# Performance work log

Hardware: AMD Instinct MI355X
Metric: run time of the kernel (lower is better)

The kernel has to match this reference:

```python
import jax, jax.numpy as jnp
import numpy as np

D = 512
V = 32000
T = 2048
B = 4
R = 8          # n_rules
STEPS = 5      # ca_steps
GATE_SCALE = 0.001  # gate_mode='micro'
EPS = 1e-5


def _layer_norm(x, g, b):
    m = jnp.mean(x, axis=-1, keepdims=True)
    v = jnp.mean((x - m) ** 2, axis=-1, keepdims=True)
    return (x - m) * jax.lax.rsqrt(v + EPS) * g + b


def setup_inputs() -> dict:
    key = jax.random.key(0)
    ks = jax.random.split(key, 16)
    s_in = 1.0 / np.sqrt(3 * D)
    s_h = 1.0 / np.sqrt(2 * D)
    s_d = 1.0 / np.sqrt(D)
    return {
        "tokens": jax.random.randint(ks[0], (B, T), 0, V, dtype=jnp.int64),
        "gate_signal": jax.random.normal(ks[1], (1, T, D), dtype=jnp.float32),
        "embed": jax.random.normal(ks[2], (V, D), dtype=jnp.float32),
        "pos_embed": jax.random.normal(ks[3], (T, D), dtype=jnp.float32),
        "rule_w1": jax.random.normal(ks[4], (R, 3 * D, 2 * D), dtype=jnp.float32) * s_in,
        "rule_b1": jnp.zeros((R, 2 * D), dtype=jnp.float32),
        "rule_w2": jax.random.normal(ks[5], (R, 2 * D, D), dtype=jnp.float32) * s_h,
        "rule_b2": jnp.zeros((R, D), dtype=jnp.float32),
        "sel_w": jax.random.normal(ks[6], (D, R), dtype=jnp.float32) * s_d,
        "sel_b": jnp.zeros((R,), dtype=jnp.float32),
        "norm_g": jnp.ones((STEPS, D), dtype=jnp.float32),
        "norm_b": jnp.zeros((STEPS, D), dtype=jnp.float32),
        "lnf_g": jnp.ones((D,), dtype=jnp.float32),
        "lnf_b": jnp.zeros((D,), dtype=jnp.float32),
        "head_w": jax.random.normal(ks[7], (D, V), dtype=jnp.float32) * s_d,
    }


def reference(tokens, gate_signal, embed, pos_embed, rule_w1, rule_b1,
              rule_w2, rule_b2, sel_w, sel_b, norm_g, norm_b,
              lnf_g, lnf_b, head_w):
    # x = token embed + positional embed  -> [B,T,D]
    x = embed[tokens] + pos_embed[None, :, :]

    # rule selector: step-invariant in 'micro' mode -> [T,R]
    logits = (gate_signal[0] * GATE_SCALE) @ sel_w + sel_b
    rw = jax.nn.softmax(logits, axis=-1)  # [T,R]

    for step in range(STEPS):
        x_left = jnp.roll(x, 1, axis=1)   # cat([x[:,-1:], x[:,:-1]])
        x_right = jnp.roll(x, -1, axis=1)  # cat([x[:,1:], x[:,:1]])
        nb = jnp.concatenate([x, x_left, x_right], axis=-1)  # [B,T,3D]
        # all R rule MLPs batched
        h = jnp.einsum('btk,rkh->btrh', nb, rule_w1) + rule_b1  # [B,T,R,2D]
        h = jax.nn.gelu(h, approximate=False)
        ro = jnp.einsum('btrh,rhd->btrd', h, rule_w2) + rule_b2  # [B,T,R,D]
        evolved = jnp.einsum('btrd,tr->btd', ro, rw)
        x = _layer_norm(x + evolved, norm_g[step], norm_b[step])

    return _layer_norm(x, lnf_g, lnf_b) @ head_w  # [B,T,V]
```

## Files before the change

kernel.cpp:

```cpp
#include <hip/hip_runtime.h>

#define T_SEQ 2048
#define BT    8192
#define DM    512
#define NR    8
#define NSTEP 5
#define K1    1536
#define H2    1024
#define VSZ   32000
#define HN    8192

using ushort_t = unsigned short;
using bf16x8 = __attribute__((ext_vector_type(8))) __bf16;
using f32x4  = __attribute__((ext_vector_type(4))) float;

__device__ __forceinline__ ushort_t f2bf(float f) {
    union { float f; unsigned u; } v; v.f = f;
    unsigned r = v.u + 0x7FFFu + ((v.u >> 16) & 1u);
    return (ushort_t)(r >> 16);
}

__device__ __forceinline__ float bf2f(unsigned hi) {
    union { unsigned u; float f; } v; v.u = hi << 16;
    return v.f;
}

__device__ __forceinline__ void gload16(const void* g, void* l) {
    __builtin_amdgcn_global_load_lds((const __attribute__((address_space(1))) void*)g,
                                     (__attribute__((address_space(3))) void*)l, 16, 0, 0);
}

__device__ __forceinline__ float gelu_fast(float x) {
    float x2 = x * x;
    float u  = x * fmaf(x2, 0.10294456f, 2.3022861f);
    float e  = exp2f(-u);
    return x * __builtin_amdgcn_rcpf(1.0f + e);
}

#define BAR()    __builtin_amdgcn_s_barrier()
#define VMCNT4() asm volatile("s_waitcnt vmcnt(4)" ::: "memory")
#define VMCNT0() asm volatile("s_waitcnt vmcnt(0)" ::: "memory")

__global__ void transpose_f32_bf16(const float* __restrict__ src, ushort_t* __restrict__ dst,
                                   int K, int N, long long srcBatch, long long dstBatch, int dstRow)
{
    __shared__ float tile[32][33];
    src += (size_t)blockIdx.z * srcBatch;
    dst += (size_t)blockIdx.z * dstBatch;
    int n0 = blockIdx.x * 32, k0 = blockIdx.y * 32;
    int tx = threadIdx.x, ty = threadIdx.y;
    #pragma unroll
    for (int i = 0; i < 32; i += 8)
        tile[ty + i][tx] = src[(size_t)(k0 + ty + i) * N + (n0 + tx)];
    __syncthreads();
    #pragma unroll
    for (int i = 0; i < 32; i += 8)
        dst[(size_t)(n0 + ty + i) * dstRow + (k0 + tx)] = f2bf(tile[tx][ty + i]);
}

__global__ void embed_pos(const int* __restrict__ tokens, const float* __restrict__ emb,
                          const float* __restrict__ pos, float* __restrict__ x,
                          ushort_t* __restrict__ xbf)
{
    int row = blockIdx.x;
    int t = row & (T_SEQ - 1);
    int tok = tokens[row];
    int i = threadIdx.x;
    float2 e = ((const float2*)(emb + (size_t)tok * DM))[i];
    float2 p = ((const float2*)(pos + (size_t)t * DM))[i];
    float2 v = make_float2(e.x + p.x, e.y + p.y);
    ((float2*)(x + (size_t)row * DM))[i] = v;
    ushort_t bb[2] = { f2bf(v.x), f2bf(v.y) };
    ((unsigned*)(xbf + (size_t)row * DM))[i] = *(const unsigned*)bb;
}

__global__ void rw_kernel(const float* __restrict__ gate, const float* __restrict__ selw,
                          const float* __restrict__ selb, const float* __restrict__ b2,
                          float* __restrict__ rw, float* __restrict__ b2rw)
{
    int t = blockIdx.x, lane = threadIdx.x;
    float p[NR];
    #pragma unroll
    for (int r = 0; r < NR; ++r) p[r] = 0.f;
    for (int d = lane; d < DM; d += 64) {
        float gv = gate[(size_t)t * DM + d] * 0.001f;
        const float* swr = selw + (size_t)d * NR;
        #pragma unroll
        for (int r = 0; r < NR; ++r) p[r] += gv * swr[r];
    }
    #pragma unroll
    for (int o = 32; o; o >>= 1) {
        #pragma unroll
        for (int r = 0; r < NR; ++r) p[r] += __shfl_xor(p[r], o, 64);
    }
    float mx = -1e30f;
    #pragma unroll
    for (int r = 0; r < NR; ++r) { p[r] += selb[r]; mx = fmaxf(mx, p[r]); }
    float s = 0.f;
    #pragma unroll
    for (int r = 0; r < NR; ++r) { p[r] = expf(p[r] - mx); s += p[r]; }
    float inv = 1.0f / s;
    #pragma unroll
    for (int r = 0; r < NR; ++r) p[r] *= inv;
    if (lane < NR) rw[t * NR + lane] = p[lane];
    #pragma unroll
    for (int it = 0; it < DM / 64; ++it) {
        int d = it * 64 + lane;
        float a = 0.f;
        #pragma unroll
        for (int r = 0; r < NR; ++r) a += p[r] * b2[r * DM + d];
        b2rw[(size_t)t * DM + d] = a;
    }
}

template<int MODE>
__global__ __launch_bounds__(256)
void ln_kernel(const float* __restrict__ xin, const ushort_t* __restrict__ evp,
               const float* __restrict__ b2rw,
               const float* __restrict__ g, const float* __restrict__ b,
               const float* __restrict__ fg, const float* __restrict__ fb,
               float* __restrict__ xout, ushort_t* __restrict__ xbf)
{
    int row = (blockIdx.x << 2) + (threadIdx.x >> 6);
    int lane = threadIdx.x & 63;
    int t = row & (T_SEQ - 1);
    int d0 = lane << 3;

    float s[8];
    {
        float4 a = *(const float4*)(xin + (size_t)row * DM + d0);
        float4 c = *(const float4*)(xin + (size_t)row * DM + d0 + 4);
        s[0]=a.x; s[1]=a.y; s[2]=a.z; s[3]=a.w; s[4]=c.x; s[5]=c.y; s[6]=c.z; s[7]=c.w;
    }
    #pragma unroll
    for (int sl = 0; sl < 4; ++sl) {
        uint4 u = *(const uint4*)(evp + ((size_t)sl * BT + row) * DM + d0);
        const unsigned w[4] = { u.x, u.y, u.z, u.w };
        #pragma unroll
        for (int j = 0; j < 4; ++j) {
            s[2*j]   += bf2f(w[j] & 0xffffu);
            s[2*j+1] += bf2f(w[j] >> 16);
        }
    }
    {
        float4 a = *(const float4*)(b2rw + (size_t)t * DM + d0);
        float4 c = *(const float4*)(b2rw + (size_t)t * DM + d0 + 4);
        s[0]+=a.x; s[1]+=a.y; s[2]+=a.z; s[3]+=a.w; s[4]+=c.x; s[5]+=c.y; s[6]+=c.z; s[7]+=c.w;
    }
    float sum = 0.f, sq = 0.f;
    #pragma unroll
    for (int j = 0; j < 8; ++j) { sum += s[j]; sq += s[j] * s[j]; }
    #pragma unroll
    for (int o = 32; o; o >>= 1) { sum += __shfl_xor(sum, o, 64); sq += __shfl_xor(sq, o, 64); }
    float mean = sum * (1.0f / DM);
    float var  = sq * (1.0f / DM) - mean * mean;
    float rstd = rsqrtf(var + 1e-5f);

    float o8[8];
    #pragma unroll
    for (int j = 0; j < 8; ++j)
        o8[j] = (s[j] - mean) * rstd * g[d0 + j] + b[d0 + j];

    if constexpr (MODE == 0) {
        float4 w0 = make_float4(o8[0], o8[1], o8[2], o8[3]);
        float4 w1 = make_float4(o8[4], o8[5], o8[6], o8[7]);
        *(float4*)(xout + (size_t)row * DM + d0) = w0;
        *(float4*)(xout + (size_t)row * DM + d0 + 4) = w1;
        ushort_t bb[8];
        #pragma unroll
        for (int j = 0; j < 8; ++j) bb[j] = f2bf(o8[j]);
        *(uint4*)(xbf + (size_t)row * DM + d0) = *(const uint4*)bb;
    } else {
        float sum2 = 0.f, sq2 = 0.f;
        #pragma unroll
        for (int j = 0; j < 8; ++j) { sum2 += o8[j]; sq2 += o8[j] * o8[j]; }
        #pragma unroll
        for (int o = 32; o; o >>= 1) { sum2 += __shfl_xor(sum2, o, 64); sq2 += __shfl_xor(sq2, o, 64); }
        float m2 = sum2 * (1.0f / DM);
        float v2 = sq2 * (1.0f / DM) - m2 * m2;
        float r2 = rsqrtf(v2 + 1e-5f);
        ushort_t bb[8];
        #pragma unroll
        for (int j = 0; j < 8; ++j)
            bb[j] = f2bf((o8[j] - m2) * r2 * fg[d0 + j] + fb[d0 + j]);
        *(uint4*)(xbf + (size_t)row * DM + d0) = *(const uint4*)bb;
    }
}

template<int EPI, int AMODE>
__global__ __launch_bounds__(512, 2)
void gemm8(const ushort_t* __restrict__ A, const ushort_t* __restrict__ Bt,
           float* __restrict__ Cf, ushort_t* __restrict__ Cb,
           int nTmG, int nTnG, int gridTn, int nPerSlice, int ktiles, int nTnTot,
           int lda, int ldb, int ldc, long long sliceC,
           const float* __restrict__ bias, const float* __restrict__ rwp)
{
    __shared__ ushort_t As[2][256 * 64];
    __shared__ ushort_t Bs[2][256 * 64];

    const int tid  = threadIdx.x;
    const int wave = tid >> 6, lane = tid & 63;
    const int wm = wave >> 2, wn = wave & 3;

    int nwg = gridDim.x, bid = blockIdx.x;
    int qq = nwg >> 3, rr = nwg & 7, xc = bid & 7, wi = bid >> 3;
    int wgid = (xc < rr ? xc * (qq + 1) : rr * (qq + 1) + (xc - rr) * qq) + wi;
    int slice = wgid / nPerSlice, rem = wgid - slice * nPerSlice;
    int gsz = nTmG * nTnG;
    int g = rem / gsz, li = rem - g * gsz;
    int gTn = g % gridTn, gTm = g / gridTn;
    int tm = gTm * nTmG + li / nTnG;
    int tn = gTn * nTnG + li % nTnG;
    if (tn >= nTnTot) return;

    const int rowBase = tm * 256, colBase = tn * 256;
    const int kbase = slice * ktiles;
    if (EPI == 0) Cf += (long long)slice * sliceC;
    if (EPI == 2) Cb += (long long)slice * sliceC;

    const int lr  = lane >> 3;
    const int skE = (((lane & 7) ^ (lr & 7)) << 3);
    const ushort_t* Bsrc = Bt + (size_t)(colBase + wave * 32 + lr) * ldb + skE;
    const ushort_t* Asrc = A + (size_t)(rowBase + wave * 32 + lr) * lda + skE;

    auto stageA = [&](int t) {
        ushort_t* d = &As[t & 1][wave * 32 * 64];
        if (AMODE == 0) {
            const ushort_t* s = Asrc + (size_t)(kbase + t) * 64;
            #pragma unroll
            for (int j = 0; j < 4; ++j)
                gload16(s + (size_t)(j * 8) * lda, d + j * 512);
        } else {
            int seg  = t >> 3;
            int dts  = (seg == 0) ? 0 : (seg == 1 ? (T_SEQ - 1) : 1);
            int colE = ((t & 7) << 6) + skE;
            #pragma unroll
            for (int j = 0; j < 4; ++j) {
                int gr = rowBase + wave * 32 + j * 8 + lr;
                int sr = (gr & ~(T_SEQ - 1)) | ((gr + dts) & (T_SEQ - 1));
                gload16(A + (size_t)sr * DM + colE, d + j * 512);
            }
        }
    };
    auto stageB = [&](int t) {
        ushort_t* d = &Bs[t & 1][wave * 32 * 64];
        const ushort_t* s = Bsrc + (size_t)(kbase + t) * 64;
        #pragma unroll
        for (int j = 0; j < 4; ++j)
            gload16(s + (size_t)(j * 8) * ldb, d + j * 512);
    };

    const int l15 = lane & 15;
    const int sl0 = (((lane >> 4) ^ (lane & 7))) << 3;
    const int sl1 = (((lane >> 4) + 4) ^ (lane & 7)) << 3;
    const int aoff = (wm * 128 + l15) * 64;
    const int boff = (wn * 64 + l15) * 64;

    f32x4 acc[8][4] = {};
    bf16x8 Ar[2][2][4];
    bf16x8 Br[2][2][2];

    auto readAall = [&](int buf) {
        #pragma unroll
        for (int mh = 0; mh < 2; ++mh)
            #pragma unroll
            for (int m = 0; m < 4; ++m) {
                int base = aoff + mh * 4096 + m * 1024;
                Ar[mh][0][m] = *(const bf16x8*)&As[buf][base + sl0];
                Ar[mh][1][m] = *(const bf16x8*)&As[buf][base + sl1];
            }
    };
    auto readB = [&](int buf, int nh) {
        #pragma unroll
        for (int n = 0; n < 2; ++n) {
            int base = boff + nh * 2048 + n * 1024;
            Br[nh][0][n] = *(const bf16x8*)&Bs[buf][base + sl0];
            Br[nh][1][n] = *(const bf16x8*)&Bs[buf][base + sl1];
        }
    };
    auto mmaQ = [&](int mh, int nh) {
        #pragma unroll
        for (int k = 0; k < 2; ++k)
            #pragma unroll
            for (int m = 0; m < 4; ++m)
                #pragma unroll
                for (int n = 0; n < 2; ++n)
                    acc[mh * 4 + m][nh * 2 + n] = __builtin_amdgcn_mfma_f32_16x16x32_bf16(
                        Ar[mh][k][m], Br[nh][k][n], acc[mh * 4 + m][nh * 2 + n], 0, 0, 0);
    };

    stageA(0); stageB(0);
    if (ktiles > 1) stageA(1);
    VMCNT4();
    BAR();

    for (int t = 0; t < ktiles; ++t) {
        const int cur = t & 1;
        readAall(cur); readB(cur, 0);
        if (t + 1 < ktiles) stageB(t + 1);
        BAR();
        __builtin_amdgcn_s_setprio(1); mmaQ(0, 0); __builtin_amdgcn_s_setprio(0);
        BAR();
        readB(cur, 1);
        bool pre = (t + 2 < ktiles);
        if (pre) stageA(t + 2);
        BAR();
        __builtin_amdgcn_s_setprio(1); mmaQ(0, 1); __builtin_amdgcn_s_setprio(0);
        BAR();
        __builtin_amdgcn_s_setprio(1); mmaQ(1, 1); mmaQ(1, 0); __builtin_amdgcn_s_setprio(0);
        if (pre) { VMCNT4(); } else { VMCNT0(); }
        BAR();
    }

    const int cl = l15, rl = (lane >> 4) << 2;
    if constexpr (EPI == 0) {
        #pragma unroll
        for (int mf = 0; mf < 8; ++mf) {
            int gr = rowBase + wm * 128 + mf * 16 + rl;
            #pragma unroll
            for (int nf = 0; nf < 4; ++nf) {
                int gc = colBase + wn * 64 + nf * 16 + cl;
                #pragma unroll
                for (int i = 0; i < 4; ++i)
                    Cf[(size_t)(gr + i) * ldc + gc] = acc[mf][nf][i];
            }
        }
    } else if constexpr (EPI == 2) {
        #pragma unroll
        for (int mf = 0; mf < 8; ++mf) {
            int gr = rowBase + wm * 128 + mf * 16 + rl;
            #pragma unroll
            for (int nf = 0; nf < 4; ++nf) {
                int gc = colBase + wn * 64 + nf * 16 + cl;
                #pragma unroll
                for (int i = 0; i < 4; ++i)
                    Cb[(size_t)(gr + i) * ldc + gc] = f2bf(acc[mf][nf][i]);
            }
        }
    } else {
        int r = (colBase + wn * 64) >> 10;
        float bv[4];
        #pragma unroll
        for (int nf = 0; nf < 4; ++nf)
            bv[nf] = bias[r * H2 + ((colBase + wn * 64 + nf * 16 + cl) & (H2 - 1))];
        #pragma unroll
        for (int mf = 0; mf < 8; ++mf) {
            int gr = rowBase + wm * 128 + mf * 16 + rl;
            #pragma unroll
            for (int i = 0; i < 4; ++i) {
                float rwv = rwp[((gr + i) & (T_SEQ - 1)) * NR + r];
                #pragma unroll
                for (int nf = 0; nf < 4; ++nf) {
                    int gc = colBase + wn * 64 + nf * 16 + cl;
                    float v = acc[mf][nf][i] + bv[nf];
                    v = gelu_fast(v) * rwv;
                    Cb[(size_t)(gr + i) * ldc + gc] = f2bf(v);
                }
            }
        }
    }
}

extern "C" void kernel_launch(void* const* d_in, const int* in_sizes, int n_in,
                              void* d_out, int out_size, void* d_ws, size_t ws_size,
                              hipStream_t stream)
{
    const int*   tokens = (const int*)d_in[0];
    const float* gate   = (const float*)d_in[1];
    const float* emb    = (const float*)d_in[2];
    const float* pos    = (const float*)d_in[3];
    const float* w1     = (const float*)d_in[4];
    const float* b1     = (const float*)d_in[5];
    const float* w2     = (const float*)d_in[6];
    const float* b2     = (const float*)d_in[7];
    const float* selw   = (const float*)d_in[8];
    const float* selb   = (const float*)d_in[9];
    const float* ng     = (const float*)d_in[10];
    const float* nbm    = (const float*)d_in[11];
    const float* lnfg   = (const float*)d_in[12];
    const float* lnfb   = (const float*)d_in[13];
    const float* headw  = (const float*)d_in[14];
    float* out = (float*)d_out;
    (void)in_sizes; (void)n_in; (void)out_size; (void)ws_size;

    size_t off = 0;
    auto alloc = [&](size_t bytes) {
        void* p = (char*)d_ws + off;
        off += (bytes + 255) & ~(size_t)255;
        return p;
    };
    float*    x    = (float*)alloc((size_t)BT * DM * 4);
    ushort_t* xbf  = (ushort_t*)alloc((size_t)BT * DM * 2);
    ushort_t* evp  = (ushort_t*)alloc((size_t)4 * BT * DM * 2);
    ushort_t* W1t  = (ushort_t*)alloc((size_t)NR * H2 * K1 * 2);
    ushort_t* W2t  = (ushort_t*)alloc((size_t)DM * HN * 2);
    ushort_t* HWt  = (ushort_t*)alloc((size_t)VSZ * DM * 2);
    float*    rw   = (float*)alloc((size_t)T_SEQ * NR * 4);
    float*    b2rw = (float*)alloc((size_t)T_SEQ * DM * 4);
    ushort_t* H    = (ushort_t*)alloc((size_t)BT * HN * 2);

    transpose_f32_bf16<<<dim3(H2 / 32, K1 / 32, NR), dim3(32, 8), 0, stream>>>(
        w1, W1t, K1, H2, (long long)K1 * H2, (long long)H2 * K1, K1);
    transpose_f32_bf16<<<dim3(DM / 32, H2 / 32, NR), dim3(32, 8), 0, stream>>>(
        w2, W2t, H2, DM, (long long)H2 * DM, (long long)H2, HN);
    transpose_f32_bf16<<<dim3(VSZ / 32, DM / 32, 1), dim3(32, 8), 0, stream>>>(
        headw, HWt, DM, VSZ, 0LL, 0LL, DM);

    embed_pos<<<dim3(BT), dim3(256), 0, stream>>>(tokens, emb, pos, x, xbf);
    rw_kernel<<<dim3(T_SEQ), dim3(64), 0, stream>>>(gate, selw, selb, b2, rw, b2rw);

    for (int s = 0; s < NSTEP; ++s) {
        gemm8<1, 1><<<dim3(1024), dim3(512), 0, stream>>>(
            xbf, W1t, nullptr, H, 32, 1, 32,
            1024, K1 / 64, 32,
            DM, K1, HN, 0LL, b1, rw);
        gemm8<2, 0><<<dim3(256), dim3(512), 0, stream>>>(
            H, W2t, nullptr, evp, 32, 2, 1,
            64, HN / 64 / 4, 2,
            HN, HN, DM, (long long)BT * DM, nullptr, nullptr);
        if (s < NSTEP - 1) {
            ln_kernel<0><<<dim3(BT / 4), dim3(256), 0, stream>>>(
                x, evp, b2rw, ng + s * DM, nbm + s * DM, nullptr, nullptr, x, xbf);
        } else {
            ln_kernel<2><<<dim3(BT / 4), dim3(256), 0, stream>>>(
                x, evp, b2rw, ng + s * DM, nbm + s * DM, lnfg, lnfb, nullptr, xbf);
        }
    }

    gemm8<0, 0><<<dim3(4096), dim3(512), 0, stream>>>(
        xbf, HWt, out, nullptr, 8, 4, 32,
        4096, DM / 64, 125,
        DM, DM, VSZ, 0LL, nullptr, nullptr);
}
```

Baseline: 1.948 ms.

## Replace 256x256 GEMM tiles with 128x128 tiles and simpler double-buffered pipeline

```diff
diff --git a/kernel.cpp b/kernel.cpp
--- a/kernel.cpp
+++ b/kernel.cpp
@@ -38,8 +38,9 @@
 }
 
 #define BAR()    __builtin_amdgcn_s_barrier()
-#define VMCNT4() asm volatile("s_waitcnt vmcnt(4)" ::: "memory")
+#define VMCNT8() asm volatile("s_waitcnt vmcnt(8)" ::: "memory")
 #define VMCNT0() asm volatile("s_waitcnt vmcnt(0)" ::: "memory")
+#define LGKM0()  asm volatile("s_waitcnt lgkmcnt(0)" ::: "memory")
 
 __global__ void transpose_f32_bf16(const float* __restrict__ src, ushort_t* __restrict__ dst,
                                    int K, int N, long long srcBatch, long long dstBatch, int dstRow)
@@ -133,7 +134,7 @@
         s[0]=a.x; s[1]=a.y; s[2]=a.z; s[3]=a.w; s[4]=c.x; s[5]=c.y; s[6]=c.z; s[7]=c.w;
     }
     #pragma unroll
-    for (int sl = 0; sl < 4; ++sl) {
+    for (int sl = 0; sl < 2; ++sl) {
         uint4 u = *(const uint4*)(evp + ((size_t)sl * BT + row) * DM + d0);
         const unsigned w[4] = { u.x, u.y, u.z, u.w };
         #pragma unroll
@@ -188,32 +189,30 @@
 }
 
 template<int EPI, int AMODE>
-__global__ __launch_bounds__(512, 2)
-void gemm8(const ushort_t* __restrict__ A, const ushort_t* __restrict__ Bt,
-           float* __restrict__ Cf, ushort_t* __restrict__ Cb,
-           int nTmG, int nTnG, int gridTn, int nPerSlice, int ktiles, int nTnTot,
-           int lda, int ldb, int ldc, long long sliceC,
-           const float* __restrict__ bias, const float* __restrict__ rwp)
-{
-    __shared__ ushort_t As[2][256 * 64];
-    __shared__ ushort_t Bs[2][256 * 64];
+__global__ __launch_bounds__(256, 2)
+void gemm128(const ushort_t* __restrict__ A, const ushort_t* __restrict__ Bt,
+             float* __restrict__ Cf, ushort_t* __restrict__ Cb,
+             int nTmG, int gridTn, int nPerSlice, int ktiles,
+             int lda, int ldb, int ldc, long long sliceC,
+             const float* __restrict__ bias, const float* __restrict__ rwp)
+{
+    __shared__ ushort_t As[2][128 * 64];
+    __shared__ ushort_t Bs[2][128 * 64];
 
     const int tid  = threadIdx.x;
     const int wave = tid >> 6, lane = tid & 63;
-    const int wm = wave >> 2, wn = wave & 3;
+    const int wm = wave >> 1, wn = wave & 1;
 
     int nwg = gridDim.x, bid = blockIdx.x;
     int qq = nwg >> 3, rr = nwg & 7, xc = bid & 7, wi = bid >> 3;
     int wgid = (xc < rr ? xc * (qq + 1) : rr * (qq + 1) + (xc - rr) * qq) + wi;
     int slice = wgid / nPerSlice, rem = wgid - slice * nPerSlice;
-    int gsz = nTmG * nTnG;
-    int g = rem / gsz, li = rem - g * gsz;
+    int g = rem / nTmG, li = rem - g * nTmG;
     int gTn = g % gridTn, gTm = g / gridTn;
-    int tm = gTm * nTmG + li / nTnG;
-    int tn = gTn * nTnG + li % nTnG;
-    if (tn >= nTnTot) return;
-
-    const int rowBase = tm * 256, colBase = tn * 256;
+    int tm = gTm * nTmG + li;
+    int tn = gTn;
+
+    const int rowBase = tm * 128, colBase = tn * 128;
     const int kbase = slice * ktiles;
     if (EPI == 0) Cf += (long long)slice * sliceC;
     if (EPI == 2) Cb += (long long)slice * sliceC;
@@ -253,70 +252,53 @@
     const int l15 = lane & 15;
     const int sl0 = (((lane >> 4) ^ (lane & 7))) << 3;
     const int sl1 = (((lane >> 4) + 4) ^ (lane & 7)) << 3;
-    const int aoff = (wm * 128 + l15) * 64;
+    const int aoff = (wm * 64 + l15) * 64;
     const int boff = (wn * 64 + l15) * 64;
 
-    f32x4 acc[8][4] = {};
-    bf16x8 Ar[2][2][4];
-    bf16x8 Br[2][2][2];
-
-    auto readAall = [&](int buf) {
-        #pragma unroll
-        for (int mh = 0; mh < 2; ++mh)
-            #pragma unroll
-            for (int m = 0; m < 4; ++m) {
-                int base = aoff + mh * 4096 + m * 1024;
-                Ar[mh][0][m] = *(const bf16x8*)&As[buf][base + sl0];
-                Ar[mh][1][m] = *(const bf16x8*)&As[buf][base + sl1];
-            }
-    };
-    auto readB = [&](int buf, int nh) {
-        #pragma unroll
-        for (int n = 0; n < 2; ++n) {
-            int base = boff + nh * 2048 + n * 1024;
-            Br[nh][0][n] = *(const bf16x8*)&Bs[buf][base + sl0];
-            Br[nh][1][n] = *(const bf16x8*)&Bs[buf][base + sl1];
-        }
-    };
-    auto mmaQ = [&](int mh, int nh) {
+    f32x4 acc[4][4] = {};
+    bf16x8 Ar[2][4], Br[2][4];
+
+    stageA(0); stageB(0);
+    if (ktiles > 1) { stageA(1); stageB(1); VMCNT8(); } else { VMCNT0(); }
+    BAR();
+
+    for (int t = 0; t < ktiles; ++t) {
+        const int cur = t & 1;
+        #pragma unroll
+        for (int m = 0; m < 4; ++m) {
+            int base = aoff + m * 1024;
+            Ar[0][m] = *(const bf16x8*)&As[cur][base + sl0];
+            Ar[1][m] = *(const bf16x8*)&As[cur][base + sl1];
+        }
+        #pragma unroll
+        for (int n = 0; n < 4; ++n) {
+            int base = boff + n * 1024;
+            Br[0][n] = *(const bf16x8*)&Bs[cur][base + sl0];
+            Br[1][n] = *(const bf16x8*)&Bs[cur][base + sl1];
+        }
+        LGKM0();
+        BAR();
+        const bool pre = (t + 2 < ktiles);
+        if (pre) { stageA(t + 2); stageB(t + 2); }
+        __builtin_amdgcn_s_setprio(1);
         #pragma unroll
         for (int k = 0; k < 2; ++k)
             #pragma unroll
             for (int m = 0; m < 4; ++m)
                 #pragma unroll
-                for (int n = 0; n < 2; ++n)
-                    acc[mh * 4 + m][nh * 2 + n] = __builtin_amdgcn_mfma_f32_16x16x32_bf16(
-                        Ar[mh][k][m], Br[nh][k][n], acc[mh * 4 + m][nh * 2 + n], 0, 0, 0);
-    };
-
-    stageA(0); stageB(0);
-    if (ktiles > 1) stageA(1);
-    VMCNT4();
-    BAR();
-
-    for (int t = 0; t < ktiles; ++t) {
-        const int cur = t & 1;
-        readAall(cur); readB(cur, 0);
-        if (t + 1 < ktiles) stageB(t + 1);
-        BAR();
-        __builtin_amdgcn_s_setprio(1); mmaQ(0, 0); __builtin_amdgcn_s_setprio(0);
-        BAR();
-        readB(cur, 1);
-        bool pre = (t + 2 < ktiles);
-        if (pre) stageA(t + 2);
-        BAR();
-        __builtin_amdgcn_s_setprio(1); mmaQ(0, 1); __builtin_amdgcn_s_setprio(0);
-        BAR();
-        __builtin_amdgcn_s_setprio(1); mmaQ(1, 1); mmaQ(1, 0); __builtin_amdgcn_s_setprio(0);
-        if (pre) { VMCNT4(); } else { VMCNT0(); }
+                for (int n = 0; n < 4; ++n)
+                    acc[m][n] = __builtin_amdgcn_mfma_f32_16x16x32_bf16(
+                        Ar[k][m], Br[k][n], acc[m][n], 0, 0, 0);
+        __builtin_amdgcn_s_setprio(0);
+        if (pre) { VMCNT8(); } else { VMCNT0(); }
         BAR();
     }
 
     const int cl = l15, rl = (lane >> 4) << 2;
     if constexpr (EPI == 0) {
         #pragma unroll
-        for (int mf = 0; mf < 8; ++mf) {
-            int gr = rowBase + wm * 128 + mf * 16 + rl;
+        for (int mf = 0; mf < 4; ++mf) {
+            int gr = rowBase + wm * 64 + mf * 16 + rl;
             #pragma unroll
             for (int nf = 0; nf < 4; ++nf) {
                 int gc = colBase + wn * 64 + nf * 16 + cl;
@@ -327,8 +309,8 @@
         }
     } else if constexpr (EPI == 2) {
         #pragma unroll
-        for (int mf = 0; mf < 8; ++mf) {
-            int gr = rowBase + wm * 128 + mf * 16 + rl;
+        for (int mf = 0; mf < 4; ++mf) {
+            int gr = rowBase + wm * 64 + mf * 16 + rl;
             #pragma unroll
             for (int nf = 0; nf < 4; ++nf) {
                 int gc = colBase + wn * 64 + nf * 16 + cl;
@@ -344,8 +326,8 @@
         for (int nf = 0; nf < 4; ++nf)
             bv[nf] = bias[r * H2 + ((colBase + wn * 64 + nf * 16 + cl) & (H2 - 1))];
         #pragma unroll
-        for (int mf = 0; mf < 8; ++mf) {
-            int gr = rowBase + wm * 128 + mf * 16 + rl;
+        for (int mf = 0; mf < 4; ++mf) {
+            int gr = rowBase + wm * 64 + mf * 16 + rl;
             #pragma unroll
             for (int i = 0; i < 4; ++i) {
                 float rwv = rwp[((gr + i) & (T_SEQ - 1)) * NR + r];
@@ -391,7 +373,7 @@
     };
     float*    x    = (float*)alloc((size_t)BT * DM * 4);
     ushort_t* xbf  = (ushort_t*)alloc((size_t)BT * DM * 2);
-    ushort_t* evp  = (ushort_t*)alloc((size_t)4 * BT * DM * 2);
+    ushort_t* evp  = (ushort_t*)alloc((size_t)2 * BT * DM * 2);
     ushort_t* W1t  = (ushort_t*)alloc((size_t)NR * H2 * K1 * 2);
     ushort_t* W2t  = (ushort_t*)alloc((size_t)DM * HN * 2);
     ushort_t* HWt  = (ushort_t*)alloc((size_t)VSZ * DM * 2);
@@ -410,13 +392,13 @@
     rw_kernel<<<dim3(T_SEQ), dim3(64), 0, stream>>>(gate, selw, selb, b2, rw, b2rw);
 
     for (int s = 0; s < NSTEP; ++s) {
-        gemm8<1, 1><<<dim3(1024), dim3(512), 0, stream>>>(
-            xbf, W1t, nullptr, H, 32, 1, 32,
-            1024, K1 / 64, 32,
+        gemm128<1, 1><<<dim3(4096), dim3(256), 0, stream>>>(
+            xbf, W1t, nullptr, H, 64, 64,
+            4096, K1 / 64,
             DM, K1, HN, 0LL, b1, rw);
-        gemm8<2, 0><<<dim3(256), dim3(512), 0, stream>>>(
-            H, W2t, nullptr, evp, 32, 2, 1,
-            64, HN / 64 / 4, 2,
+        gemm128<2, 0><<<dim3(512), dim3(256), 0, stream>>>(
+            H, W2t, nullptr, evp, 64, 4,
+            256, HN / 64 / 2,
             HN, HN, DM, (long long)BT * DM, nullptr, nullptr);
         if (s < NSTEP - 1) {
             ln_kernel<0><<<dim3(BT / 4), dim3(256), 0, stream>>>(
@@ -427,8 +409,8 @@
         }
     }
 
-    gemm8<0, 0><<<dim3(4096), dim3(512), 0, stream>>>(
-        xbf, HWt, out, nullptr, 8, 4, 32,
-        4096, DM / 64, 125,
+    gemm128<0, 0><<<dim3(16000), dim3(256), 0, stream>>>(
+        xbf, HWt, out, nullptr, 64, 250,
+        16000, DM / 64,
         DM, DM, VSZ, 0LL, nullptr, nullptr);
 }
```

Result: slower. 2.376 ms (+21.9%).
